# Performance work log

Measured on AMD Instinct MI355X. Metric: run time of the kernel, lower is better.

The kernel has to match this reference:

```python
import jax, jax.numpy as jnp
import numpy as np
from jax import lax

T, B, I, H, FC, O = 2048, 64, 128, 128, 32, 2

def _xavier(key, shape):
    # torch xavier_normal_ on [..., fan_out, fan_in]
    std = float(np.sqrt(2.0 / (shape[-2] + shape[-1])))
    return jax.random.normal(key, shape, jnp.float32) * std

def setup_inputs() -> dict:
    key = jax.random.key(0)
    ks = jax.random.split(key, 16)
    inp = {
        'x': jax.random.normal(ks[0], (T, B, I), jnp.float32),
        'w_ig': _xavier(ks[1], (B, H, I)),
        'w_ii': _xavier(ks[2], (B, H, I)),
        'w_if': _xavier(ks[3], (B, H, I)),
        'w_io': _xavier(ks[4], (B, H, I)),
        'w_hg': _xavier(ks[5], (B, H, H)),
        'w_hi': _xavier(ks[6], (B, H, H)),
        'w_hf': _xavier(ks[7], (B, H, H)),
        'w_ho': _xavier(ks[8], (B, H, H)),
        'b_g': jnp.zeros((B, H, 1), jnp.float32),
        'b_i': jnp.zeros((B, H, 1), jnp.float32),
        'b_f': jnp.zeros((B, H, 1), jnp.float32),
        'b_o': jnp.zeros((B, H, 1), jnp.float32),
        'fc1_w': _xavier(ks[9], (FC, H)),
        'fc1_b': jnp.zeros((FC,), jnp.float32),
        'fc2_w': _xavier(ks[10], (O, FC)),
        'fc2_b': jnp.zeros((O,), jnp.float32),
    }
    return inp

def reference(x, w_ig, w_ii, w_if, w_io, w_hg, w_hi, w_hf, w_ho,
              b_g, b_i, b_f, b_o, fc1_w, fc1_b, fc2_w, fc2_b):
    b, h = w_hg.shape[0], w_hg.shape[1]
    # Original bug: gates read self.hidd which is never updated -> stays zeros.
    hidd0 = jnp.zeros((b, h), x.dtype)
    # Recurrent contributions (identically zero, kept for faithfulness)
    rg = jnp.einsum('bhk,bk->bh', w_hg, hidd0)
    ri = jnp.einsum('bhk,bk->bh', w_hi, hidd0)
    rf = jnp.einsum('bhk,bk->bh', w_hf, hidd0)
    ro = jnp.einsum('bhk,bk->bh', w_ho, hidd0)
    # Input gate pre-activations for all timesteps in one einsum each: [T,B,H]
    g = jnp.tanh(jnp.einsum('bhi,tbi->tbh', w_ig, x) + rg + b_g[:, :, 0])
    i_ = jax.nn.sigmoid(jnp.einsum('bhi,tbi->tbh', w_ii, x) + ri + b_i[:, :, 0])
    f = jax.nn.sigmoid(jnp.einsum('bhi,tbi->tbh', w_if, x) + rf + b_f[:, :, 0])
    o = jax.nn.sigmoid(jnp.einsum('bhi,tbi->tbh', w_io, x) + ro + b_o[:, :, 0])

    def step(carry, gifo):
        c, _ = carry
        g_t, i_t, f_t, o_t = gifo
        c = f_t * c + i_t * g_t
        hid = o_t * jnp.tanh(c)
        return (c, hid), None

    c0 = jnp.zeros((b, h), x.dtype)
    (c_fin, h_fin), _ = lax.scan(step, (c0, c0), (g, i_, f, o))
    # classifier on last hidden: Linear -> tanh -> Linear -> log_softmax
    z = jnp.tanh(h_fin @ fc1_w.T + fc1_b) @ fc2_w.T + fc2_b
    return jax.nn.log_softmax(z, axis=1)
```

## Files before the change

### kernel.cpp

```cpp
#include <hip/hip_runtime.h>
#include <hip/hip_bf16.h>
#include <cstddef>

#define T_DIM 2048
#define B_DIM 64
#define I_DIM 128
#define H_DIM 128
#define FC_DIM 32
#define O_DIM 2

#define NC 16
#define TC (T_DIM / NC)
#define MT 8
#define CPB 2

#define LOG2E  1.44269504088896f
#define LOG2E2 2.88539008177793f

typedef __attribute__((ext_vector_type(8))) short bf16x8;
typedef __attribute__((ext_vector_type(4))) float f32x4;

__device__ __forceinline__ bf16x8 cvt8(const float* __restrict__ p) {
    union { bf16x8 v; __hip_bfloat162 h2[4]; } u;
#pragma unroll
    for (int j = 0; j < 4; ++j) {
        float2 f2 = {p[2 * j], p[2 * j + 1]};
        u.h2[j] = __float22bfloat162_rn(f2);
    }
    return u.v;
}

__global__ void convert_w_kernel(const float* __restrict__ wg,
                                 const float* __restrict__ wi,
                                 const float* __restrict__ wf,
                                 short* __restrict__ og,
                                 short* __restrict__ oi,
                                 short* __restrict__ of)
{
    const float* src = (blockIdx.y == 0) ? wg : (blockIdx.y == 1) ? wi : wf;
    short* dst       = (blockIdx.y == 0) ? og : (blockIdx.y == 1) ? oi : of;
    const float scale = (blockIdx.y == 0) ? LOG2E2 : LOG2E;
    const size_t idx = ((size_t)blockIdx.x * 256 + threadIdx.x) * 8;
    float4 u0 = *(const float4*)(src + idx);
    float4 u1 = *(const float4*)(src + idx + 4);
    float a[8] = {u0.x * scale, u0.y * scale, u0.z * scale, u0.w * scale,
                  u1.x * scale, u1.y * scale, u1.z * scale, u1.w * scale};
    *(bf16x8*)(dst + idx) = cvt8(a);
}

__global__ __launch_bounds__(512, 4)
void gates_scan_kernel(const float* __restrict__ x,
    const short* __restrict__ wg, const short* __restrict__ wi,
    const short* __restrict__ wf,
    const float* __restrict__ b_g, const float* __restrict__ b_i,
    const float* __restrict__ b_f,
    float* __restrict__ wsF, float* __restrict__ wsA)
{
    __shared__ short frag[MT * 4 * 64 * 8];

    const int L    = threadIdx.x & 63;
    const int wv   = threadIdx.x >> 6;
    const int col  = L & 15;
    const int quad = L >> 4;
    const int bid  = blockIdx.x;
    const int b    = bid & (B_DIM - 1);
    const int cp   = bid >> 6;

    const int h = wv * 16 + col;
    bf16x8 Bg[4], Bi[4], Bf[4];
    {
        const size_t wo = ((size_t)b * H_DIM + h) * I_DIM + quad * 8;
#pragma unroll
        for (int kk = 0; kk < 4; ++kk) {
            Bg[kk] = *(const bf16x8*)(wg + wo + kk * 32);
            Bi[kk] = *(const bf16x8*)(wi + wo + kk * 32);
            Bf[kk] = *(const bf16x8*)(wf + wo + kk * 32);
        }
    }
    const float biasg = b_g[b * H_DIM + h] * LOG2E2;
    const float biasi = b_i[b * H_DIM + h] * LOG2E;
    const float biasf = b_f[b * H_DIM + h] * LOG2E;

    const int tl = (col >> 2) * 32 + wv * 4 + (col & 3);

    {
        const float* xp = x + ((size_t)(cp * CPB * TC + tl) * B_DIM + b) * I_DIM;
#pragma unroll
        for (int kk = 0; kk < 4; ++kk) {
            const int i0 = quad * 8 + kk * 32;
            float4 u0 = *(const float4*)(xp + i0);
            float4 u1 = *(const float4*)(xp + i0 + 4);
            float a[8] = {u0.x, u0.y, u0.z, u0.w, u1.x, u1.y, u1.z, u1.w};
            *(bf16x8*)(frag + (((wv * 4 + kk) * 64) + L) * 8) = cvt8(a);
        }
    }
    __syncthreads();

    float4 px[8];

#pragma unroll
    for (int j = 0; j < CPB; ++j) {
        const int c = cp * CPB + j;

        if (j + 1 < CPB) {
            const float* xp = x + ((size_t)((c + 1) * TC + tl) * B_DIM + b) * I_DIM;
#pragma unroll
            for (int kk = 0; kk < 4; ++kk) {
                const int i0 = quad * 8 + kk * 32;
                px[2 * kk]     = *(const float4*)(xp + i0);
                px[2 * kk + 1] = *(const float4*)(xp + i0 + 4);
            }
        }

        float Fq = 1.0f, Aq = 0.0f;
#pragma unroll 2
        for (int mt = 0; mt < MT; ++mt) {
            bf16x8 ah[4];
#pragma unroll
            for (int kk = 0; kk < 4; ++kk)
                ah[kk] = *(const bf16x8*)(frag + (((mt * 4 + kk) * 64) + L) * 8);
            f32x4 accg = {0.f, 0.f, 0.f, 0.f};
            f32x4 acci = {0.f, 0.f, 0.f, 0.f};
            f32x4 accf = {0.f, 0.f, 0.f, 0.f};
#pragma unroll
            for (int kk = 0; kk < 4; ++kk) {
                accg = __builtin_amdgcn_mfma_f32_16x16x32_bf16(ah[kk], Bg[kk], accg, 0, 0, 0);
                acci = __builtin_amdgcn_mfma_f32_16x16x32_bf16(ah[kk], Bi[kk], acci, 0, 0, 0);
                accf = __builtin_amdgcn_mfma_f32_16x16x32_bf16(ah[kk], Bf[kk], accf, 0, 0, 0);
            }
#pragma unroll
            for (int r = 0; r < 4; ++r) {
                float g  = 2.0f * __builtin_amdgcn_rcpf(
                               1.0f + __builtin_amdgcn_exp2f(-(accg[r] + biasg))) - 1.0f;
                float iv = __builtin_amdgcn_rcpf(
                               1.0f + __builtin_amdgcn_exp2f(-(acci[r] + biasi)));
                float fv = __builtin_amdgcn_rcpf(
                               1.0f + __builtin_amdgcn_exp2f(-(accf[r] + biasf)));
                Aq = fv * Aq + iv * g;
                Fq = fv * Fq;
            }
        }

        float Fo = __shfl_xor(Fq, 16, 64);
        float Ao = __shfl_xor(Aq, 16, 64);
        if ((quad & 1) == 0) { Aq = Fo * Aq + Ao; Fq = Fo * Fq; }
        else                 { Aq = Fq * Ao + Aq; Fq = Fq * Fo; }
        Fo = __shfl_xor(Fq, 32, 64);
        Ao = __shfl_xor(Aq, 32, 64);
        if (quad < 2) { Aq = Fo * Aq + Ao; Fq = Fo * Fq; }
        else          { Aq = Fq * Ao + Aq; Fq = Fq * Fo; }

        if (quad == 0) {
            const int idx = (b * NC + c) * H_DIM + h;
            wsF[idx] = Fq;
            wsA[idx] = Aq;
        }

        if (j + 1 < CPB) {
            __syncthreads();
#pragma unroll
            for (int kk = 0; kk < 4; ++kk) {
                float a[8] = {px[2 * kk].x,     px[2 * kk].y,
                              px[2 * kk].z,     px[2 * kk].w,
                              px[2 * kk + 1].x, px[2 * kk + 1].y,
                              px[2 * kk + 1].z, px[2 * kk + 1].w};
                *(bf16x8*)(frag + (((wv * 4 + kk) * 64) + L) * 8) = cvt8(a);
            }
            __syncthreads();
        }
    }
}

__global__ void finish_kernel(const float* __restrict__ x,
    const float* __restrict__ w_io, const float* __restrict__ b_o,
    const float* __restrict__ fc1_w, const float* __restrict__ fc1_b,
    const float* __restrict__ fc2_w, const float* __restrict__ fc2_b,
    const float* __restrict__ wsF, const float* __restrict__ wsA,
    float* __restrict__ out)
{
    const int b = blockIdx.x;
    const int h = threadIdx.x;
    __shared__ float hf[H_DIM];
    __shared__ float z1[FC_DIM];

    float c = 0.0f;
#pragma unroll
    for (int nc = 0; nc < NC; ++nc) {
        const int idx = (b * NC + nc) * H_DIM + h;
        c = wsF[idx] * c + wsA[idx];
    }
    const float* xl = x + ((size_t)(T_DIM - 1) * B_DIM + b) * I_DIM;
    const float* wo = w_io + ((size_t)b * H_DIM + h) * I_DIM;
    float acc = b_o[b * H_DIM + h];
#pragma unroll 8
    for (int i = 0; i < I_DIM; i += 4) {
        float4 xa = *(const float4*)(xl + i);
        float4 wa = *(const float4*)(wo + i);
        acc += xa.x * wa.x + xa.y * wa.y + xa.z * wa.z + xa.w * wa.w;
    }
    const float o = 1.0f / (1.0f + expf(-acc));
    hf[h] = o * tanhf(c);
    __syncthreads();

    if (h < FC_DIM) {
        float a = fc1_b[h];
        const float* w1 = fc1_w + h * H_DIM;
        for (int i = 0; i < H_DIM; ++i) a += w1[i] * hf[i];
        z1[h] = tanhf(a);
    }
    __syncthreads();

    if (h == 0) {
        float z0 = fc2_b[0], zo1 = fc2_b[1];
        for (int j = 0; j < FC_DIM; ++j) {
            z0  += fc2_w[j] * z1[j];
            zo1 += fc2_w[FC_DIM + j] * z1[j];
        }
        const float m = fmaxf(z0, zo1);
        const float lse = m + logf(expf(z0 - m) + expf(zo1 - m));
        out[b * O_DIM + 0] = z0 - lse;
        out[b * O_DIM + 1] = zo1 - lse;
    }
}

extern "C" void kernel_launch(void* const* d_in, const int* in_sizes, int n_in,
                              void* d_out, int out_size, void* d_ws, size_t ws_size,
                              hipStream_t stream) {
    const float* x     = (const float*)d_in[0];
    const float* w_ig  = (const float*)d_in[1];
    const float* w_ii  = (const float*)d_in[2];
    const float* w_if  = (const float*)d_in[3];
    const float* w_io  = (const float*)d_in[4];
    const float* b_g   = (const float*)d_in[9];
    const float* b_i   = (const float*)d_in[10];
    const float* b_f   = (const float*)d_in[11];
    const float* b_o   = (const float*)d_in[12];
    const float* fc1_w = (const float*)d_in[13];
    const float* fc1_b = (const float*)d_in[14];
    const float* fc2_w = (const float*)d_in[15];
    const float* fc2_b = (const float*)d_in[16];

    const size_t NW = (size_t)B_DIM * H_DIM * I_DIM;
    short* wgc = (short*)d_ws;
    short* wic = wgc + NW;
    short* wfc = wic + NW;
    float* wsF = (float*)(wfc + NW);
    float* wsA = wsF + (size_t)B_DIM * NC * H_DIM;
    float* out = (float*)d_out;

    convert_w_kernel<<<dim3(NW / (256 * 8), 3), 256, 0, stream>>>(
        w_ig, w_ii, w_if, wgc, wic, wfc);

    gates_scan_kernel<<<dim3(B_DIM * NC / CPB), 512, 0, stream>>>(
        x, wgc, wic, wfc, b_g, b_i, b_f, wsF, wsA);

    finish_kernel<<<B_DIM, 128, 0, stream>>>(x, w_io, b_o, fc1_w, fc1_b,
                                             fc2_w, fc2_b, wsF, wsA, out);
}
```

Before: 160.4 us.

## Double-buffer x fragments in LDS and split scan into finer time chunks

The time axis is now split into 32 chunks of 64 steps instead of 16 chunks of 128, and each block handles 4 chunks instead of 2, so the grid size stays the same. The LDS fragment buffer is doubled so the next chunk's x tile can be written while the current one is read, which drops one __syncthreads per chunk. Each wave now stages only half the k-slices of a smaller tile, and the mt loop is fully unrolled. The finish kernel has to combine twice as many chunk partials, and register pressure from the full unroll may change.

```diff
diff --git a/kernel.cpp b/kernel.cpp
--- a/kernel.cpp
+++ b/kernel.cpp
@@ -9,10 +9,10 @@
 #define FC_DIM 32
 #define O_DIM 2
 
-#define NC 16
+#define NC 32
 #define TC (T_DIM / NC)
-#define MT 8
-#define CPB 2
+#define MT 4
+#define CPB 4
 
 #define LOG2E  1.44269504088896f
 #define LOG2E2 2.88539008177793f
@@ -56,7 +56,7 @@
     const float* __restrict__ b_f,
     float* __restrict__ wsF, float* __restrict__ wsA)
 {
-    __shared__ short frag[MT * 4 * 64 * 8];
+    __shared__ short frag[2][MT * 4 * 64 * 8];
 
     const int L    = threadIdx.x & 63;
     const int wv   = threadIdx.x >> 6;
@@ -66,6 +66,10 @@
     const int b    = bid & (B_DIM - 1);
     const int cp   = bid >> 6;
 
+    const int mt_s = wv >> 1;
+    const int kk0  = (wv & 1) * 2;
+    const int tl_s = (col >> 2) * 16 + mt_s * 4 + (col & 3);
+
     const int h = wv * 16 + col;
     bf16x8 Bg[4], Bi[4], Bf[4];
     {
@@ -81,44 +85,44 @@
     const float biasi = b_i[b * H_DIM + h] * LOG2E;
     const float biasf = b_f[b * H_DIM + h] * LOG2E;
 
-    const int tl = (col >> 2) * 32 + wv * 4 + (col & 3);
-
     {
-        const float* xp = x + ((size_t)(cp * CPB * TC + tl) * B_DIM + b) * I_DIM;
-#pragma unroll
-        for (int kk = 0; kk < 4; ++kk) {
+        const float* xp = x + ((size_t)(cp * CPB * TC + tl_s) * B_DIM + b) * I_DIM;
+#pragma unroll
+        for (int kq = 0; kq < 2; ++kq) {
+            const int kk = kk0 + kq;
             const int i0 = quad * 8 + kk * 32;
             float4 u0 = *(const float4*)(xp + i0);
             float4 u1 = *(const float4*)(xp + i0 + 4);
             float a[8] = {u0.x, u0.y, u0.z, u0.w, u1.x, u1.y, u1.z, u1.w};
-            *(bf16x8*)(frag + (((wv * 4 + kk) * 64) + L) * 8) = cvt8(a);
+            *(bf16x8*)(&frag[0][(((mt_s * 4 + kk) * 64) + L) * 8]) = cvt8(a);
         }
     }
     __syncthreads();
 
-    float4 px[8];
+    float4 px[4];
 
 #pragma unroll
     for (int j = 0; j < CPB; ++j) {
         const int c = cp * CPB + j;
+        const short* fr = frag[j & 1];
 
         if (j + 1 < CPB) {
-            const float* xp = x + ((size_t)((c + 1) * TC + tl) * B_DIM + b) * I_DIM;
-#pragma unroll
-            for (int kk = 0; kk < 4; ++kk) {
-                const int i0 = quad * 8 + kk * 32;
-                px[2 * kk]     = *(const float4*)(xp + i0);
-                px[2 * kk + 1] = *(const float4*)(xp + i0 + 4);
+            const float* xp = x + ((size_t)((c + 1) * TC + tl_s) * B_DIM + b) * I_DIM;
+#pragma unroll
+            for (int kq = 0; kq < 2; ++kq) {
+                const int i0 = quad * 8 + (kk0 + kq) * 32;
+                px[2 * kq]     = *(const float4*)(xp + i0);
+                px[2 * kq + 1] = *(const float4*)(xp + i0 + 4);
             }
         }
 
         float Fq = 1.0f, Aq = 0.0f;
-#pragma unroll 2
+#pragma unroll
         for (int mt = 0; mt < MT; ++mt) {
             bf16x8 ah[4];
 #pragma unroll
             for (int kk = 0; kk < 4; ++kk)
-                ah[kk] = *(const bf16x8*)(frag + (((mt * 4 + kk) * 64) + L) * 8);
+                ah[kk] = *(const bf16x8*)(fr + (((mt * 4 + kk) * 64) + L) * 8);
             f32x4 accg = {0.f, 0.f, 0.f, 0.f};
             f32x4 acci = {0.f, 0.f, 0.f, 0.f};
             f32x4 accf = {0.f, 0.f, 0.f, 0.f};
@@ -157,14 +161,15 @@
         }
 
         if (j + 1 < CPB) {
-            __syncthreads();
-#pragma unroll
-            for (int kk = 0; kk < 4; ++kk) {
-                float a[8] = {px[2 * kk].x,     px[2 * kk].y,
-                              px[2 * kk].z,     px[2 * kk].w,
-                              px[2 * kk + 1].x, px[2 * kk + 1].y,
-                              px[2 * kk + 1].z, px[2 * kk + 1].w};
-                *(bf16x8*)(frag + (((wv * 4 + kk) * 64) + L) * 8) = cvt8(a);
+            short* fw = frag[(j + 1) & 1];
+#pragma unroll
+            for (int kq = 0; kq < 2; ++kq) {
+                const int kk = kk0 + kq;
+                float a[8] = {px[2 * kq].x,     px[2 * kq].y,
+                              px[2 * kq].z,     px[2 * kq].w,
+                              px[2 * kq + 1].x, px[2 * kq + 1].y,
+                              px[2 * kq + 1].z, px[2 * kq + 1].w};
+                *(bf16x8*)(fw + (((mt_s * 4 + kk) * 64) + L) * 8) = cvt8(a);
             }
             __syncthreads();
         }
```

After: 158.6 us. Within noise of the previous version (-1.1%).
